# Optimization experiments

Measured on AMD Instinct MI355X. Metric: run time of the kernel, lower is better.

## Reference

```python
import jax, jax.numpy as jnp
import numpy as np

B, NP, N, C, H = 16, 512, 1024, 1024, 16
HD = C // H
HID = 4 * C
EPS = 1e-5


def _layernorm(x, g, b):
    mu = jnp.mean(x, axis=-1, keepdims=True)
    var = jnp.mean(jnp.square(x - mu), axis=-1, keepdims=True)
    return (x - mu) * jax.lax.rsqrt(var + EPS) * g + b


def setup_inputs() -> dict:
    key = jax.random.key(0)
    ks = jax.random.split(key, 12)
    x = jax.random.normal(ks[0], (B, NP, C), dtype=jnp.float32)
    cache_k = jax.random.normal(ks[1], (B, H, N, HD), dtype=jnp.float32)
    cache_v = jax.random.normal(ks[2], (B, H, N, HD), dtype=jnp.float32)
    # update_mask: exactly NP active (to-be-updated) token slots per batch row
    scores = jax.random.uniform(ks[3], (B, N))
    top = jnp.argsort(scores, axis=1)[:, :NP]
    update_mask = jnp.zeros((B, N), dtype=bool).at[jnp.arange(B)[:, None], top].set(True)
    s = 0.02
    qkv_w = jax.random.normal(ks[4], (C, 3 * C), dtype=jnp.float32) * s
    qkv_b = jnp.zeros((3 * C,), dtype=jnp.float32)
    proj_w = jax.random.normal(ks[5], (C, C), dtype=jnp.float32) * s
    proj_b = jnp.zeros((C,), dtype=jnp.float32)
    n1_g = jnp.ones((C,), dtype=jnp.float32)
    n1_b = jnp.zeros((C,), dtype=jnp.float32)
    n2_g = jnp.ones((C,), dtype=jnp.float32)
    n2_b = jnp.zeros((C,), dtype=jnp.float32)
    fc1_w = jax.random.normal(ks[6], (C, HID), dtype=jnp.float32) * s
    fc1_b = jnp.zeros((HID,), dtype=jnp.float32)
    fc2_w = jax.random.normal(ks[7], (HID, C), dtype=jnp.float32) * s
    fc2_b = jnp.zeros((C,), dtype=jnp.float32)
    return dict(x=x, cache_k=cache_k, cache_v=cache_v, update_mask=update_mask,
                qkv_w=qkv_w, qkv_b=qkv_b, proj_w=proj_w, proj_b=proj_b,
                n1_g=n1_g, n1_b=n1_b, n2_g=n2_g, n2_b=n2_b,
                fc1_w=fc1_w, fc1_b=fc1_b, fc2_w=fc2_w, fc2_b=fc2_b)


def reference(x, cache_k, cache_v, update_mask, qkv_w, qkv_b, proj_w, proj_b,
              n1_g, n1_b, n2_g, n2_b, fc1_w, fc1_b, fc2_w, fc2_b):
    Bq, Np, Cd = x.shape
    h = _layernorm(x, n1_g, n1_b)
    qkv = (h @ qkv_w + qkv_b).reshape(Bq, Np, 3, H, HD)
    q, k, v = jnp.moveaxis(qkv, 2, 0)               # each [B, Np, H, HD]
    q = jnp.swapaxes(q, 1, 2)                       # [B, H, Np, HD]
    k = jnp.swapaxes(k, 1, 2)
    v = jnp.swapaxes(v, 1, 2)
    # masked_scatter_: i-th new token -> i-th masked slot (row-uniform mask count)
    idx = jnp.argsort(jnp.logical_not(update_mask), axis=1)[:, :Np]  # [B, Np]
    k_full = jax.vmap(lambda c, i, kn: c.at[:, i, :].set(kn))(cache_k, idx, k)
    v_full = jax.vmap(lambda c, i, vn: c.at[:, i, :].set(vn))(cache_v, idx, v)
    scale = HD ** -0.5
    attn = jnp.einsum('bhqd,bhkd->bhqk', q * scale, k_full)  # [B,H,Np,N]
    attn = jax.nn.softmax(attn, axis=-1)
    o = jnp.einsum('bhqk,bhkd->bhqd', attn, v_full)
    o = jnp.swapaxes(o, 1, 2).reshape(Bq, Np, Cd)
    o = o @ proj_w + proj_b
    x = x + o
    h2 = _layernorm(x, n2_g, n2_b)
    mlp = jax.nn.gelu(h2 @ fc1_w + fc1_b, approximate=False) @ fc2_w + fc2_b
    return x + mlp
```

## Files before the change

### kernel.cpp

```cpp
#include <hip/hip_runtime.h>
#include <hip/hip_bf16.h>
#include <math.h>

#define Bd   16
#define NPd  512
#define Nd   1024
#define Cd   1024
#define Hd   16
#define HDd  64
#define HIDd 4096
#define EPSd 1e-5f
#define MRd  (Bd * NPd)

typedef unsigned short u16;
typedef __bf16 bf16x8 __attribute__((ext_vector_type(8)));
typedef float  f32x4  __attribute__((ext_vector_type(4)));

__device__ __forceinline__ u16 f2bf(float f) {
    unsigned int u = __builtin_bit_cast(unsigned int, f);
    u = u + 0x7fffu + ((u >> 16) & 1u);
    return (u16)(u >> 16);
}

__device__ __forceinline__ void async_load16(const void* g, void* l) {
    __builtin_amdgcn_global_load_lds(
        (const __attribute__((address_space(1))) void*)(uintptr_t)g,
        (__attribute__((address_space(3))) void*)(unsigned int)(uintptr_t)l,
        16, 0, 0);
}

__global__ __launch_bounds__(256) void build_src(const void* __restrict__ mask_raw,
                                                 int* __restrict__ src) {
    const int b = blockIdx.x;
    const int t = threadIdx.x;
    const unsigned char* m8 = (const unsigned char*)mask_raw;
    const int* m32 = (const int*)mask_raw;

    int c = 0;
    #pragma unroll
    for (int i = 0; i < 4; i++) c += (m8[b * Nd + t * 4 + i] != 0) ? 1 : 0;
    #pragma unroll
    for (int off = 1; off < 64; off <<= 1) c += __shfl_xor(c, off);
    __shared__ int warr[4];
    if ((t & 63) == 0) warr[t >> 6] = c;
    __syncthreads();
    const int c8 = warr[0] + warr[1] + warr[2] + warr[3];
    const bool use8 = (c8 == NPd);

    int f[4];
    #pragma unroll
    for (int i = 0; i < 4; i++) {
        const int n = t * 4 + i;
        f[i] = use8 ? (m8[b * Nd + n] != 0) : (m32[b * Nd + n] != 0);
    }
    const int loc = f[0] + f[1] + f[2] + f[3];

    int sc_ = loc;
    #pragma unroll
    for (int off = 1; off < 64; off <<= 1) {
        const int u = __shfl_up(sc_, off);
        if ((t & 63) >= off) sc_ += u;
    }
    __shared__ int wtot[4];
    __syncthreads();
    if ((t & 63) == 63) wtot[t >> 6] = sc_;
    __syncthreads();
    int base = 0;
    for (int w = 0; w < (t >> 6); w++) base += wtot[w];

    int run = base + sc_ - loc;
    #pragma unroll
    for (int i = 0; i < 4; i++) {
        const int n = t * 4 + i;
        src[b * Nd + n] = f[i] ? run : -1;
        run += f[i];
    }
}

__global__ __launch_bounds__(256) void ln_kernel(const float* __restrict__ x,
                                                 const float* __restrict__ g,
                                                 const float* __restrict__ bb,
                                                 u16* __restrict__ out) {
    const int row = blockIdx.x;
    const int t = threadIdx.x;
    const float* xr = x + (size_t)row * Cd;
    const float4 v = *(const float4*)(xr + t * 4);
    float s = v.x + v.y + v.z + v.w;
    float q = v.x * v.x + v.y * v.y + v.z * v.z + v.w * v.w;
    #pragma unroll
    for (int off = 1; off < 64; off <<= 1) {
        s += __shfl_xor(s, off);
        q += __shfl_xor(q, off);
    }
    __shared__ float ss[4], qq[4];
    if ((t & 63) == 0) { ss[t >> 6] = s; qq[t >> 6] = q; }
    __syncthreads();
    s = ss[0] + ss[1] + ss[2] + ss[3];
    q = qq[0] + qq[1] + qq[2] + qq[3];
    const float mu = s * (1.0f / Cd);
    const float var = q * (1.0f / Cd) - mu * mu;
    const float rs = rsqrtf(var + EPSd);
    const float4 gv = *(const float4*)(g + t * 4);
    const float4 bv = *(const float4*)(bb + t * 4);
    ushort4 r;
    r.x = f2bf((v.x - mu) * rs * gv.x + bv.x);
    r.y = f2bf((v.y - mu) * rs * gv.y + bv.y);
    r.z = f2bf((v.z - mu) * rs * gv.z + bv.z);
    r.w = f2bf((v.w - mu) * rs * gv.w + bv.w);
    *(ushort4*)(out + (size_t)row * Cd + t * 4) = r;
}

__global__ __launch_bounds__(256) void conv_t(const float* __restrict__ W,
                                              u16* __restrict__ Wt,
                                              int K, int N) {
    __shared__ float tile[32][33];
    const int k0 = blockIdx.y * 32;
    const int n0 = blockIdx.x * 32;
    const int t = threadIdx.x;
    const int row = t >> 3, c4 = (t & 7) * 4;
    const float4 v = *(const float4*)(W + (size_t)(k0 + row) * N + n0 + c4);
    tile[row][c4 + 0] = v.x;
    tile[row][c4 + 1] = v.y;
    tile[row][c4 + 2] = v.z;
    tile[row][c4 + 3] = v.w;
    __syncthreads();
    ushort4 o;
    o.x = f2bf(tile[c4 + 0][row]);
    o.y = f2bf(tile[c4 + 1][row]);
    o.z = f2bf(tile[c4 + 2][row]);
    o.w = f2bf(tile[c4 + 3][row]);
    *(ushort4*)(Wt + (size_t)(n0 + row) * K + k0 + c4) = o;
}

template <int EPI, typename OUT_T>
__global__ __launch_bounds__(256) void gemm_mfma(const u16* __restrict__ A,
                                                 const u16* __restrict__ Wt,
                                                 const float* __restrict__ bias,
                                                 const float* __restrict__ res,
                                                 OUT_T* __restrict__ out,
                                                 int K, int Nn) {
    __shared__ u16 As[3][128 * 32];
    __shared__ u16 Bs[3][128 * 32];

    const int t = threadIdx.x;
    const int L = t & 63;
    const int w = t >> 6;
    const int wm = w >> 1, wn = w & 1;

    const int gx = gridDim.x;
    const int nwg = gx * gridDim.y;
    int id = blockIdx.y * gx + blockIdx.x;
    id = (id & 7) * (nwg >> 3) + (id >> 3);
    const int m0 = (id / gx) * 128;
    const int n0 = (id % gx) * 128;

    const int srow = 32 * w + (L >> 2);
    const int scol = (((L & 3) ^ ((L >> 3) & 3)) * 8);
    const u16* ap0 = A  + (size_t)(m0 + srow) * K + scol;
    const u16* ap1 = ap0 + (size_t)16 * K;
    const u16* bp0 = Wt + (size_t)(n0 + srow) * K + scol;
    const u16* bp1 = bp0 + (size_t)16 * K;

    f32x4 acc[4][4];
    const f32x4 zero = {0.f, 0.f, 0.f, 0.f};
    #pragma unroll
    for (int i = 0; i < 4; i++)
        #pragma unroll
        for (int j = 0; j < 4; j++) acc[i][j] = zero;

    const int rr = L & 15;
    const int frag_off = rr * 32 + ((((L >> 4)) ^ ((rr >> 1) & 3)) * 8);
    const int nsteps = K >> 5;

#define STAGE_G(s_, kt_) do {                                   \
        const int off_ = (kt_) << 5;                            \
        async_load16(ap0 + off_, &As[s_][w * 1024]);            \
        async_load16(ap1 + off_, &As[s_][w * 1024 + 512]);      \
        async_load16(bp0 + off_, &Bs[s_][w * 1024]);            \
        async_load16(bp1 + off_, &Bs[s_][w * 1024 + 512]);      \
    } while (0)

    STAGE_G(0, 0);
    STAGE_G(1, 1);
    asm volatile("s_waitcnt vmcnt(4)" ::: "memory");
    __builtin_amdgcn_s_barrier();

    int cur = 0;
    for (int kt = 0; kt < nsteps; kt++) {
        if (kt + 2 < nsteps) {
            int s2 = cur + 2; if (s2 >= 3) s2 -= 3;
            STAGE_G(s2, kt + 2);
        }

        bf16x8 a[4], b[4];
        #pragma unroll
        for (int i = 0; i < 4; i++) {
            a[i] = *(const bf16x8*)&As[cur][(wm * 64 + i * 16) * 32 + frag_off];
            b[i] = *(const bf16x8*)&Bs[cur][(wn * 64 + i * 16) * 32 + frag_off];
        }
        #pragma unroll
        for (int i = 0; i < 4; i++)
            #pragma unroll
            for (int j = 0; j < 4; j++)
                acc[i][j] = __builtin_amdgcn_mfma_f32_16x16x32_bf16(a[i], b[j], acc[i][j], 0, 0, 0);

        if (kt + 2 < nsteps) asm volatile("s_waitcnt vmcnt(4)" ::: "memory");
        else                 asm volatile("s_waitcnt vmcnt(0)" ::: "memory");
        __builtin_amdgcn_s_barrier();
        cur = (cur + 1 == 3) ? 0 : cur + 1;
    }
#undef STAGE_G

    const int cn = n0 + wn * 64 + (L & 15);
    const int cm = m0 + wm * 64 + (L >> 4) * 4;
    #pragma unroll
    for (int i = 0; i < 4; i++) {
        #pragma unroll
        for (int j = 0; j < 4; j++) {
            const int nn = cn + j * 16;
            const float bv = bias[nn];
            #pragma unroll
            for (int r = 0; r < 4; r++) {
                const int mm = cm + i * 16 + r;
                float v = acc[i][j][r] + bv;
                if (EPI == 2) v = 0.5f * v * (1.0f + erff(v * 0.70710678118654752f));
                if (EPI == 1) v += res[(size_t)mm * Nn + nn];
                if constexpr (sizeof(OUT_T) == 2) out[(size_t)mm * Nn + nn] = (OUT_T)f2bf(v);
                else out[(size_t)mm * Nn + nn] = v;
            }
        }
    }
}

__global__ __launch_bounds__(256) void kv_cast(const u16* __restrict__ qkv,
                                               const float* __restrict__ ck,
                                               const float* __restrict__ cv,
                                               const int* __restrict__ srcArr,
                                               u16* __restrict__ Kb,
                                               u16* __restrict__ Vtb) {
    const int id = blockIdx.x;
    const int nt = id & 15, hh = (id >> 4) & 15, b = id >> 8;
    const int t = threadIdx.x;
    __shared__ u16 Vl[64][72];

    const int row = t >> 2;
    const int dd = (t & 3) * 16;
    const int n = nt * 64 + row;
    const int sidx = srcArr[b * Nd + n];

    u16 kv16[16], vv16[16];
    if (sidx >= 0) {
        const u16* kp = qkv + (size_t)(b * NPd + sidx) * 3072 + Cd + hh * 64 + dd;
        const u16* vp = kp + Cd;
        *(ulonglong2*)&kv16[0] = *(const ulonglong2*)kp;
        *(ulonglong2*)&kv16[8] = *(const ulonglong2*)(kp + 8);
        *(ulonglong2*)&vv16[0] = *(const ulonglong2*)vp;
        *(ulonglong2*)&vv16[8] = *(const ulonglong2*)(vp + 8);
    } else {
        const float* kp = ck + ((size_t)((b * Hd + hh) * Nd + n)) * HDd + dd;
        const float* vp = cv + ((size_t)((b * Hd + hh) * Nd + n)) * HDd + dd;
        #pragma unroll
        for (int c = 0; c < 4; c++) {
            const float4 kc4 = *(const float4*)(kp + c * 4);
            const float4 vc4 = *(const float4*)(vp + c * 4);
            kv16[c * 4 + 0] = f2bf(kc4.x); kv16[c * 4 + 1] = f2bf(kc4.y);
            kv16[c * 4 + 2] = f2bf(kc4.z); kv16[c * 4 + 3] = f2bf(kc4.w);
            vv16[c * 4 + 0] = f2bf(vc4.x); vv16[c * 4 + 1] = f2bf(vc4.y);
            vv16[c * 4 + 2] = f2bf(vc4.z); vv16[c * 4 + 3] = f2bf(vc4.w);
        }
    }

    u16* ko = Kb + ((size_t)((b * Hd + hh) * Nd + n)) * HDd + dd;
    *(ulonglong2*)ko = *(ulonglong2*)&kv16[0];
    *(ulonglong2*)(ko + 8) = *(ulonglong2*)&kv16[8];

    #pragma unroll
    for (int i = 0; i < 16; i++) Vl[row][dd + i] = vv16[i];
    __syncthreads();

    const int d = t >> 2, nc = (t & 3) * 16;
    u16 ov[16];
    #pragma unroll
    for (int i = 0; i < 16; i++) ov[i] = Vl[nc + i][d];
    u16* vo = Vtb + ((size_t)((b * Hd + hh) * HDd + d)) * Nd + nt * 64 + nc;
    *(ulonglong2*)vo = *(ulonglong2*)&ov[0];
    *(ulonglong2*)(vo + 8) = *(ulonglong2*)&ov[8];
}

__global__ __launch_bounds__(256) void attn_mfma(const u16* __restrict__ qkv,
                                                 const u16* __restrict__ Kb,
                                                 const u16* __restrict__ Vtb,
                                                 u16* __restrict__ attno) {
    const int orig = blockIdx.y * 256 + blockIdx.x;
    const int xc = orig & 7, pos = orig >> 3;
    const int bh = (xc << 5) | (pos >> 3);
    const int qt = pos & 7;
    const int b = bh >> 4, hh = bh & 15;
    const int t = threadIdx.x;
    const int L = t & 63;
    const int w = t >> 6;
    const int g = L >> 4;
    const int q16 = L & 15;

    __shared__ u16 Qs[4096];
    __shared__ u16 Ks[4096];
    __shared__ u16 Vs[4096];
    __shared__ u16 Ps[4][16 * 72];

    const size_t kbase = (size_t)((b * Hd + hh) * Nd) * HDd;
    const size_t vbase = (size_t)((b * Hd + hh) * HDd) * Nd;

    #pragma unroll
    for (int j = 0; j < 2; j++) {
        const int row = 16 * w + 8 * j + (L >> 3);
        const int ch = (L & 7) ^ (row & 7);
        const u16* gq = qkv + (size_t)(b * NPd + qt * 64 + row) * 3072 + hh * 64 + ch * 8;
        async_load16(gq, Qs + (16 * w + 8 * j) * 64);
    }

    f32x4 acc[4];
    const f32x4 zero = {0.f, 0.f, 0.f, 0.f};
    #pragma unroll
    for (int nb = 0; nb < 4; nb++) acc[nb] = zero;
    float m_run = -INFINITY;
    float l_run = 0.f;

    bf16x8 aq0, aq1;

    for (int kt = 0; kt < 16; kt++) {
        __syncthreads();
        #pragma unroll
        for (int j = 0; j < 2; j++) {
            const int row = 16 * w + 8 * j + (L >> 3);
            const int ch = (L & 7) ^ (row & 7);
            async_load16(Kb + kbase + (size_t)(kt * 64 + row) * 64 + ch * 8,
                         Ks + (16 * w + 8 * j) * 64);
            async_load16(Vtb + vbase + (size_t)row * Nd + kt * 64 + ch * 8,
                         Vs + (16 * w + 8 * j) * 64);
        }
        __syncthreads();

        if (kt == 0) {
            const int qrow = 16 * w + q16;
            aq0 = *(const bf16x8*)&Qs[qrow * 64 + ((g       ^ (L & 7)) * 8)];
            aq1 = *(const bf16x8*)&Qs[qrow * 64 + (((4 + g) ^ (L & 7)) * 8)];
        }

        f32x4 s[4];
        #pragma unroll
        for (int kb = 0; kb < 4; kb++) {
            const int krow = kb * 16 + q16;
            const bf16x8 bk0 = *(const bf16x8*)&Ks[krow * 64 + ((g       ^ (L & 7)) * 8)];
            const bf16x8 bk1 = *(const bf16x8*)&Ks[krow * 64 + (((4 + g) ^ (L & 7)) * 8)];
            s[kb] = __builtin_amdgcn_mfma_f32_16x16x32_bf16(bk0, aq0, zero, 0, 0, 0);
            s[kb] = __builtin_amdgcn_mfma_f32_16x16x32_bf16(bk1, aq1, s[kb], 0, 0, 0);
        }

        float m0 = fmaxf(fmaxf(s[0][0], s[0][1]), fmaxf(s[0][2], s[0][3]));
        float m1 = fmaxf(fmaxf(s[1][0], s[1][1]), fmaxf(s[1][2], s[1][3]));
        float m2 = fmaxf(fmaxf(s[2][0], s[2][1]), fmaxf(s[2][2], s[2][3]));
        float m3 = fmaxf(fmaxf(s[3][0], s[3][1]), fmaxf(s[3][2], s[3][3]));
        float mx = fmaxf(fmaxf(m0, m1), fmaxf(m2, m3)) * 0.125f;
        mx = fmaxf(mx, __shfl_xor(mx, 16));
        mx = fmaxf(mx, __shfl_xor(mx, 32));

        if (__any(mx > m_run + 8.f)) {
            const float mn = fmaxf(m_run, mx);
            const float al = __expf(m_run - mn);
            m_run = mn;
            l_run *= al;
            float alr[4];
            #pragma unroll
            for (int r = 0; r < 4; r++) alr[r] = __shfl(al, g * 4 + r);
            #pragma unroll
            for (int nb = 0; nb < 4; nb++)
                #pragma unroll
                for (int r = 0; r < 4; r++) acc[nb][r] *= alr[r];
        }

        u16* pw = &Ps[w][0];
        float ps = 0.f;
        #pragma unroll
        for (int kb = 0; kb < 4; kb++) {
            float p0 = __expf(fmaf(s[kb][0], 0.125f, -m_run));
            float p1 = __expf(fmaf(s[kb][1], 0.125f, -m_run));
            float p2 = __expf(fmaf(s[kb][2], 0.125f, -m_run));
            float p3 = __expf(fmaf(s[kb][3], 0.125f, -m_run));
            ps += (p0 + p1) + (p2 + p3);
            ushort4 v4;
            v4.x = f2bf(p0); v4.y = f2bf(p1); v4.z = f2bf(p2); v4.w = f2bf(p3);
            *(ushort4*)&pw[q16 * 72 + kb * 16 + g * 4] = v4;
        }
        ps += __shfl_xor(ps, 16);
        ps += __shfl_xor(ps, 32);
        l_run += ps;

        const bf16x8 ap0 = *(const bf16x8*)&Ps[w][q16 * 72 +      g * 8];
        const bf16x8 ap1 = *(const bf16x8*)&Ps[w][q16 * 72 + 32 + g * 8];
        #pragma unroll
        for (int nb = 0; nb < 4; nb++) {
            const int drow = nb * 16 + q16;
            const bf16x8 bv0 = *(const bf16x8*)&Vs[drow * 64 + ((g       ^ (L & 7)) * 8)];
            const bf16x8 bv1 = *(const bf16x8*)&Vs[drow * 64 + (((4 + g) ^ (L & 7)) * 8)];
            acc[nb] = __builtin_amdgcn_mfma_f32_16x16x32_bf16(ap0, bv0, acc[nb], 0, 0, 0);
            acc[nb] = __builtin_amdgcn_mfma_f32_16x16x32_bf16(ap1, bv1, acc[nb], 0, 0, 0);
        }
    }

    const float invq = 1.0f / l_run;
    float inv[4];
    #pragma unroll
    for (int r = 0; r < 4; r++) inv[r] = __shfl(invq, g * 4 + r);
    #pragma unroll
    for (int nb = 0; nb < 4; nb++)
        #pragma unroll
        for (int r = 0; r < 4; r++) {
            const int q = qt * 64 + w * 16 + g * 4 + r;
            const int d = nb * 16 + q16;
            attno[(size_t)(b * NPd + q) * Cd + hh * 64 + d] = f2bf(acc[nb][r] * inv[r]);
        }
}

extern "C" void kernel_launch(void* const* d_in, const int* in_sizes, int n_in,
                              void* d_out, int out_size, void* d_ws, size_t ws_size,
                              hipStream_t stream) {
    const float* x       = (const float*)d_in[0];
    const float* cache_k = (const float*)d_in[1];
    const float* cache_v = (const float*)d_in[2];
    const void*  mask    = d_in[3];
    const float* qkv_w   = (const float*)d_in[4];
    const float* qkv_b   = (const float*)d_in[5];
    const float* proj_w  = (const float*)d_in[6];
    const float* proj_b  = (const float*)d_in[7];
    const float* n1_g    = (const float*)d_in[8];
    const float* n1_b    = (const float*)d_in[9];
    const float* n2_g    = (const float*)d_in[10];
    const float* n2_b    = (const float*)d_in[11];
    const float* fc1_w   = (const float*)d_in[12];
    const float* fc1_b   = (const float*)d_in[13];
    const float* fc2_w   = (const float*)d_in[14];
    const float* fc2_b   = (const float*)d_in[15];
    float* out = (float*)d_out;

    const size_t MR = (size_t)Bd * NPd;
    char* ws = (char*)d_ws;
    int*   srcArr = (int*)ws;
    float* x2     = (float*)(ws + 65536);
    u16*   h      = (u16*)(x2 + MR * Cd);
    u16*   attno  = h + MR * Cd;
    u16*   qkv    = attno + MR * Cd;
    u16*   Kb     = qkv + MR * 3 * Cd;
    u16*   Vtb    = Kb + (size_t)Bd * Hd * Nd * HDd;
    u16*   m1     = qkv;
    u16*   qkv_wt = Vtb + (size_t)Bd * Hd * Nd * HDd;
    u16*   proj_wt= qkv_wt + (size_t)3 * Cd * Cd;
    u16*   fc1_wt = proj_wt + (size_t)Cd * Cd;
    u16*   fc2_wt = fc1_wt + (size_t)Cd * HIDd;

    build_src<<<Bd, 256, 0, stream>>>(mask, srcArr);
    conv_t<<<dim3(3 * Cd / 32, Cd / 32),  256, 0, stream>>>(qkv_w,  qkv_wt,  Cd,   3 * Cd);
    conv_t<<<dim3(Cd / 32, Cd / 32),      256, 0, stream>>>(proj_w, proj_wt, Cd,   Cd);
    conv_t<<<dim3(HIDd / 32, Cd / 32),    256, 0, stream>>>(fc1_w,  fc1_wt,  Cd,   HIDd);
    conv_t<<<dim3(Cd / 32, HIDd / 32),    256, 0, stream>>>(fc2_w,  fc2_wt,  HIDd, Cd);

    ln_kernel<<<MR, 256, 0, stream>>>(x, n1_g, n1_b, h);
    gemm_mfma<0, u16><<<dim3(3 * Cd / 128, MR / 128), 256, 0, stream>>>(
        h, qkv_wt, qkv_b, nullptr, qkv, Cd, 3 * Cd);
    kv_cast<<<Bd * Hd * (Nd / 64), 256, 0, stream>>>(qkv, cache_k, cache_v, srcArr, Kb, Vtb);
    attn_mfma<<<dim3(Bd * Hd, NPd / 64), 256, 0, stream>>>(qkv, Kb, Vtb, attno);
    gemm_mfma<1, float><<<dim3(Cd / 128, MR / 128), 256, 0, stream>>>(
        attno, proj_wt, proj_b, x, x2, Cd, Cd);
    ln_kernel<<<MR, 256, 0, stream>>>(x2, n2_g, n2_b, h);
    gemm_mfma<2, u16><<<dim3(HIDd / 128, MR / 128), 256, 0, stream>>>(
        h, fc1_wt, fc1_b, nullptr, m1, Cd, HIDd);
    gemm_mfma<1, float><<<dim3(Cd / 128, MR / 128), 256, 0, stream>>>(
        m1, fc2_wt, fc2_b, x2, out, HIDd, Cd);
}
```

Before: 607.0 us.

## Double-buffer K/V tiles in attention kernel to overlap loads with MFMA

The attention kernel now keeps two shared-memory buffers for K and V and issues the async loads for the next key tile before computing on the current one. Each iteration ends with one vmcnt wait and barrier instead of two barriers around the loads. The Q fragment load is hoisted out of the loop. This hides global-load latency behind MFMA and softmax work, at the cost of extra LDS (about 16 KB more), which may lower occupancy. The attention kernel is only one part of the full block, so the effect on total time is limited.

New measurement: 597.3 us. No clear change (-1.6%).

```diff
diff --git a/kernel.cpp b/kernel.cpp
--- a/kernel.cpp
+++ b/kernel.cpp
@@ -303,20 +303,40 @@
     const int q16 = L & 15;
 
     __shared__ u16 Qs[4096];
-    __shared__ u16 Ks[4096];
-    __shared__ u16 Vs[4096];
+    __shared__ u16 Ks[2][4096];
+    __shared__ u16 Vs[2][4096];
     __shared__ u16 Ps[4][16 * 72];
 
     const size_t kbase = (size_t)((b * Hd + hh) * Nd) * HDd;
     const size_t vbase = (size_t)((b * Hd + hh) * HDd) * Nd;
 
-    #pragma unroll
-    for (int j = 0; j < 2; j++) {
-        const int row = 16 * w + 8 * j + (L >> 3);
-        const int ch = (L & 7) ^ (row & 7);
-        const u16* gq = qkv + (size_t)(b * NPd + qt * 64 + row) * 3072 + hh * 64 + ch * 8;
-        async_load16(gq, Qs + (16 * w + 8 * j) * 64);
-    }
+    const int srow0 = 16 * w + (L >> 3);
+    const int sch0  = (L & 7) ^ (srow0 & 7);
+    const int srow1 = srow0 + 8;
+    const int sch1  = (L & 7) ^ (srow1 & 7);
+
+#define STAGE_KV(buf_, kt_) do {                                              \
+        async_load16(Kb + kbase + (size_t)((kt_) * 64 + srow0) * 64 + sch0 * 8, \
+                     Ks[buf_] + (16 * w) * 64);                               \
+        async_load16(Vtb + vbase + (size_t)srow0 * Nd + (kt_) * 64 + sch0 * 8, \
+                     Vs[buf_] + (16 * w) * 64);                               \
+        async_load16(Kb + kbase + (size_t)((kt_) * 64 + srow1) * 64 + sch1 * 8, \
+                     Ks[buf_] + (16 * w + 8) * 64);                           \
+        async_load16(Vtb + vbase + (size_t)srow1 * Nd + (kt_) * 64 + sch1 * 8, \
+                     Vs[buf_] + (16 * w + 8) * 64);                           \
+    } while (0)
+
+    async_load16(qkv + (size_t)(b * NPd + qt * 64 + srow0) * 3072 + hh * 64 + sch0 * 8,
+                 Qs + (16 * w) * 64);
+    async_load16(qkv + (size_t)(b * NPd + qt * 64 + srow1) * 3072 + hh * 64 + sch1 * 8,
+                 Qs + (16 * w + 8) * 64);
+    STAGE_KV(0, 0);
+    asm volatile("s_waitcnt vmcnt(0)" ::: "memory");
+    __builtin_amdgcn_s_barrier();
+
+    const int qrow = 16 * w + q16;
+    const bf16x8 aq0 = *(const bf16x8*)&Qs[qrow * 64 + ((g       ^ (L & 7)) * 8)];
+    const bf16x8 aq1 = *(const bf16x8*)&Qs[qrow * 64 + (((4 + g) ^ (L & 7)) * 8)];
 
     f32x4 acc[4];
     const f32x4 zero = {0.f, 0.f, 0.f, 0.f};
@@ -325,33 +345,16 @@
     float m_run = -INFINITY;
     float l_run = 0.f;
 
-    bf16x8 aq0, aq1;
-
     for (int kt = 0; kt < 16; kt++) {
-        __syncthreads();
-        #pragma unroll
-        for (int j = 0; j < 2; j++) {
-            const int row = 16 * w + 8 * j + (L >> 3);
-            const int ch = (L & 7) ^ (row & 7);
-            async_load16(Kb + kbase + (size_t)(kt * 64 + row) * 64 + ch * 8,
-                         Ks + (16 * w + 8 * j) * 64);
-            async_load16(Vtb + vbase + (size_t)row * Nd + kt * 64 + ch * 8,
-                         Vs + (16 * w + 8 * j) * 64);
-        }
-        __syncthreads();
-
-        if (kt == 0) {
-            const int qrow = 16 * w + q16;
-            aq0 = *(const bf16x8*)&Qs[qrow * 64 + ((g       ^ (L & 7)) * 8)];
-            aq1 = *(const bf16x8*)&Qs[qrow * 64 + (((4 + g) ^ (L & 7)) * 8)];
-        }
+        const int cur = kt & 1;
+        if (kt < 15) STAGE_KV(cur ^ 1, kt + 1);
 
         f32x4 s[4];
         #pragma unroll
         for (int kb = 0; kb < 4; kb++) {
             const int krow = kb * 16 + q16;
-            const bf16x8 bk0 = *(const bf16x8*)&Ks[krow * 64 + ((g       ^ (L & 7)) * 8)];
-            const bf16x8 bk1 = *(const bf16x8*)&Ks[krow * 64 + (((4 + g) ^ (L & 7)) * 8)];
+            const bf16x8 bk0 = *(const bf16x8*)&Ks[cur][krow * 64 + ((g       ^ (L & 7)) * 8)];
+            const bf16x8 bk1 = *(const bf16x8*)&Ks[cur][krow * 64 + (((4 + g) ^ (L & 7)) * 8)];
             s[kb] = __builtin_amdgcn_mfma_f32_16x16x32_bf16(bk0, aq0, zero, 0, 0, 0);
             s[kb] = __builtin_amdgcn_mfma_f32_16x16x32_bf16(bk1, aq1, s[kb], 0, 0, 0);
         }
@@ -400,12 +403,16 @@
         #pragma unroll
         for (int nb = 0; nb < 4; nb++) {
             const int drow = nb * 16 + q16;
-            const bf16x8 bv0 = *(const bf16x8*)&Vs[drow * 64 + ((g       ^ (L & 7)) * 8)];
-            const bf16x8 bv1 = *(const bf16x8*)&Vs[drow * 64 + (((4 + g) ^ (L & 7)) * 8)];
+            const bf16x8 bv0 = *(const bf16x8*)&Vs[cur][drow * 64 + ((g       ^ (L & 7)) * 8)];
+            const bf16x8 bv1 = *(const bf16x8*)&Vs[cur][drow * 64 + (((4 + g) ^ (L & 7)) * 8)];
             acc[nb] = __builtin_amdgcn_mfma_f32_16x16x32_bf16(ap0, bv0, acc[nb], 0, 0, 0);
             acc[nb] = __builtin_amdgcn_mfma_f32_16x16x32_bf16(ap1, bv1, acc[nb], 0, 0, 0);
         }
-    }
+
+        asm volatile("s_waitcnt vmcnt(0)" ::: "memory");
+        __builtin_amdgcn_s_barrier();
+    }
+#undef STAGE_KV
 
     const float invq = 1.0f / l_run;
     float inv[4];
```
